# Optimization experiments

Hardware: AMD Instinct MI355X
Metric: run time of the kernel (lower is better)

The kernel has to match this reference:

```python
import jax, jax.numpy as jnp
import numpy as np
from jax import lax

EPS = 1e-5
NUM_BITS = 8          # activation quantization bits
NUM_BITS_WEIGHT = 8   # weight quantization bits


def fake_quant(x, bits):
    """Uniform min-max quantize-dequantize (per-tensor), STE on round."""
    mn = jnp.min(x)
    mx = jnp.max(x)
    scale = jnp.maximum((mx - mn) / (2 ** bits - 1), jnp.asarray(1e-8, x.dtype))
    q = jnp.round((x - mn) / scale) * scale + mn
    # straight-through estimator: identity gradient through rounding
    return x + lax.stop_gradient(q - x)


def batchnorm(x, gamma, beta, mean, var):
    # x: [N, C, H, W]; stats per channel C (eval mode, running stats)
    inv = gamma / jnp.sqrt(var + EPS)
    return x * inv[None, :, None, None] + (beta - mean * inv)[None, :, None, None]


def qconv(x, w, padding):
    xq = fake_quant(x, NUM_BITS)
    wq = fake_quant(w, NUM_BITS_WEIGHT)
    return lax.conv_general_dilated(
        xq, wq, window_strides=(1, 1), padding=padding,
        dimension_numbers=("NCHW", "OIHW", "NCHW"))


def setup_inputs() -> dict:
    key = jax.random.key(0)
    ks = jax.random.split(key, 8)
    C_in, bn_size, growth = 512, 4, 32
    C_mid = bn_size * growth  # 128
    N, H, W = 64, 28, 28
    x = jax.random.normal(ks[0], (N, C_in, H, W), dtype=jnp.float32)
    gamma1 = jax.random.uniform(ks[1], (C_in,), minval=0.5, maxval=1.5)
    beta1 = jax.random.normal(ks[2], (C_in,)) * 0.1
    mean1 = jax.random.normal(ks[3], (C_in,)) * 0.1
    var1 = jax.random.uniform(ks[4], (C_in,), minval=0.5, maxval=1.5)
    w1 = jax.random.normal(ks[5], (C_mid, C_in, 1, 1)) * (1.0 / np.sqrt(C_in))
    gamma2 = jax.random.uniform(ks[6], (C_mid,), minval=0.5, maxval=1.5)
    beta2 = jax.random.normal(ks[7], (C_mid,)) * 0.1
    mean2 = jax.random.normal(jax.random.fold_in(key, 10), (C_mid,)) * 0.1
    var2 = jax.random.uniform(jax.random.fold_in(key, 11), (C_mid,), minval=0.5, maxval=1.5)
    w2 = jax.random.normal(jax.random.fold_in(key, 12), (growth, C_mid, 3, 3)) * (1.0 / np.sqrt(C_mid * 9))
    return {"x": x, "gamma1": gamma1, "beta1": beta1, "mean1": mean1, "var1": var1,
            "w1": w1, "gamma2": gamma2, "beta2": beta2, "mean2": mean2, "var2": var2,
            "w2": w2}


def reference(x, gamma1, beta1, mean1, var1, w1, gamma2, beta2, mean2, var2, w2):
    h = jax.nn.relu(batchnorm(x, gamma1, beta1, mean1, var1))
    h = qconv(h, w1, padding=((0, 0), (0, 0)))            # 1x1 conv, 512 -> 128
    h = jax.nn.relu(batchnorm(h, gamma2, beta2, mean2, var2))
    h = qconv(h, w2, padding=((1, 1), (1, 1)))            # 3x3 conv, 128 -> 32
    # drop_rate == 0 -> dropout is identity
    return h
```

## Files before the change

kernel.cpp:

```cpp
#include <hip/hip_runtime.h>

typedef unsigned short u16;
typedef unsigned short u16x4 __attribute__((ext_vector_type(4)));
typedef unsigned short u16x8 __attribute__((ext_vector_type(8)));
typedef short bf16x8 __attribute__((ext_vector_type(8)));
typedef float f32x4 __attribute__((ext_vector_type(4)));

#define EPSF 1e-5f

#define C1   512
#define C2   128
#define C3   32
#define HH   28
#define WW   28
#define HW   784
#define NHW  50176
#define XELEMS 25690112

#define SCAN_BLOCKS 1024
#define KA_GRID     1027
#define CONV1_BLOCKS 392
#define CONV2_BLOCKS 784

#define WS_BN1I   64
#define WS_BN1B   2112
#define WS_BN2I   4160
#define WS_BN2B   4672
#define WS_WQ1    5376
#define WS_WQ2    136448
#define WS_P1     210176
#define WS_P2     226560
#define WS_H2     233472

__device__ __forceinline__ float bf2f(u16 u) { return __uint_as_float(((unsigned)u) << 16); }
__device__ __forceinline__ u16 f2bf(float f) {
  unsigned x = __float_as_uint(f);
  return (u16)((x + 0x7fffu + ((x >> 16) & 1u)) >> 16);
}
__device__ __forceinline__ float finz(float f) {
  unsigned u = __float_as_uint(f);
  return ((u & 0x7f800000u) == 0x7f800000u) ? 0.0f : f;
}

__device__ __forceinline__ void block_minmax(float& mn, float& mx) {
  for (int m = 32; m; m >>= 1) {
    mn = fminf(mn, __shfl_xor(mn, m));
    mx = fmaxf(mx, __shfl_xor(mx, m));
  }
  __shared__ float wmn[4], wmx[4];
  const int wv = threadIdx.x >> 6;
  if ((threadIdx.x & 63) == 0) { wmn[wv] = mn; wmx[wv] = mx; }
  __syncthreads();
  if (threadIdx.x == 0) {
    mn = fminf(fminf(wmn[0], wmn[1]), fminf(wmn[2], wmn[3]));
    mx = fmaxf(fmaxf(wmx[0], wmx[1]), fmaxf(wmx[2], wmx[3]));
  }
}

__global__ __launch_bounds__(256) void kA_kernel(
    const float* __restrict__ x, const float* g1, const float* be1,
    const float* m1, const float* v1, const float* w1,
    const float* g2, const float* be2, const float* m2, const float* v2,
    const float* w2, unsigned char* ws) {
  const int t = threadIdx.x;
  const int bid = blockIdx.x;
  float2* p1 = (float2*)(ws + WS_P1);
  u16* wq1 = (u16*)(ws + WS_WQ1);
  u16* wq2 = (u16*)(ws + WS_WQ2);
  __shared__ float bc[2];

  if (bid < SCAN_BLOCKS) {
    const int c = bid >> 1;
    const int n0 = (bid & 1) << 5;
    const f32x4* xb = (const f32x4*)x + ((size_t)n0 * C1 + c) * 196;
    float mn0 = 3.4e38f, mx0 = -3.4e38f, mn1 = 3.4e38f, mx1 = -3.4e38f;
    float mn2 = 3.4e38f, mx2 = -3.4e38f, mn3 = 3.4e38f, mx3 = -3.4e38f;
    auto P = [&](int j, float& mn, float& mx) {
      int s = j / 196;
      int g = j - s * 196;
      f32x4 v = xb[(size_t)s * (C1 * 196) + g];
      mn = fminf(mn, fminf(fminf(v[0], v[1]), fminf(v[2], v[3])));
      mx = fmaxf(mx, fmaxf(fmaxf(v[0], v[1]), fmaxf(v[2], v[3])));
    };
    int j = t;
    for (; j + 768 < 6272; j += 1024) {
      P(j, mn0, mx0); P(j + 256, mn1, mx1);
      P(j + 512, mn2, mx2); P(j + 768, mn3, mx3);
    }
    for (; j < 6272; j += 256) P(j, mn0, mx0);
    float mn = fminf(fminf(mn0, mn1), fminf(mn2, mn3));
    float mx = fmaxf(fmaxf(mx0, mx1), fmaxf(mx2, mx3));
    block_minmax(mn, mx);
    if (t == 0) {
      float inv = g1[c] / sqrtf(v1[c] + EPSF);
      float bb = be1[c] - m1[c] * inv;
      float lo = fmaxf(fmaf(mn, inv, bb), 0.0f);
      float hi = fmaxf(fmaf(mx, inv, bb), 0.0f);
      p1[bid] = make_float2(lo, hi);
    }
  } else if (bid == SCAN_BLOCKS) {
    const f32x4* w4 = (const f32x4*)w1;
    float mn = 3.4e38f, mx = -3.4e38f;
#pragma unroll 8
    for (int k = t; k < 16384; k += 256) {
      f32x4 v = w4[k];
#pragma unroll
      for (int j = 0; j < 4; j++) {
        float f = finz(v[j]); mn = fminf(mn, f); mx = fmaxf(mx, f);
      }
    }
    block_minmax(mn, mx);
    if (t == 0) { bc[0] = mn; bc[1] = mx; }
    __syncthreads();
    const float mnv = bc[0];
    const float s = fmaxf((bc[1] - mnv) / 255.0f, 1e-8f);
    const float rs = 1.0f / s;
#pragma unroll 4
    for (int k = t; k < 16384; k += 256) {
      f32x4 v = w4[k];
      u16x4 o;
#pragma unroll
      for (int j = 0; j < 4; j++)
        o[j] = f2bf(fmaf(rintf((finz(v[j]) - mnv) * rs), s, mnv));
      *(u16x4*)(wq1 + k * 4) = o;
    }
  } else if (bid == SCAN_BLOCKS + 1) {
    const f32x4* w4 = (const f32x4*)w2;
    float mn = 3.4e38f, mx = -3.4e38f;
#pragma unroll 4
    for (int k = t; k < 9216; k += 256) {
      f32x4 v = w4[k];
#pragma unroll
      for (int j = 0; j < 4; j++) {
        float f = finz(v[j]); mn = fminf(mn, f); mx = fmaxf(mx, f);
      }
    }
    block_minmax(mn, mx);
    if (t == 0) { bc[0] = mn; bc[1] = mx; }
    __syncthreads();
    const float mnv = bc[0];
    const float s = fmaxf((bc[1] - mnv) / 255.0f, 1e-8f);
    const float rs = 1.0f / s;
    for (int jj = t; jj < 36864; jj += 256) {
      int tap = jj >> 12;
      int rem = jj & 4095;
      float f = finz(w2[rem * 9 + tap]);
      wq2[jj] = f2bf(fmaf(rintf((f - mnv) * rs), s, mnv));
    }
  } else {
    float* bn1i = (float*)(ws + WS_BN1I);
    float* bn1b = (float*)(ws + WS_BN1B);
    float* bn2i = (float*)(ws + WS_BN2I);
    float* bn2b = (float*)(ws + WS_BN2B);
    for (int c = t; c < C1; c += 256) {
      float inv = g1[c] / sqrtf(v1[c] + EPSF);
      bn1i[c] = inv;
      bn1b[c] = be1[c] - m1[c] * inv;
    }
    if (t < C2) {
      float inv = g2[t] / sqrtf(v2[t] + EPSF);
      bn2i[t] = inv;
      bn2b[t] = be2[t] - m2[t] * inv;
    }
  }
}

__global__ __launch_bounds__(256) void conv1_kernel(const float* __restrict__ x,
                                                    unsigned char* ws) {
  const float* bn1i = (const float*)(ws + WS_BN1I);
  const float* bn1b = (const float*)(ws + WS_BN1B);
  const float* bn2i = (const float*)(ws + WS_BN2I);
  const float* bn2b = (const float*)(ws + WS_BN2B);
  const u16* wq1 = (const u16*)(ws + WS_WQ1);
  const float2* p1 = (const float2*)(ws + WS_P1);
  float2* p2 = (float2*)(ws + WS_P2);
  u16* h2 = (u16*)(ws + WS_H2);

  __shared__ __align__(16) u16 Alds[2][128 * 40];
  __shared__ __align__(16) u16 Blds[2][128 * 40];
  __shared__ float bc[2];
  __shared__ float wred[8];

  const int t = threadIdx.x;
  const int sp0 = blockIdx.x * 128;

  {
    float mn = 3.4e38f, mx = 0.0f;
    for (int i = t; i < SCAN_BLOCKS; i += 256) {
      float2 p = p1[i];
      mn = fminf(mn, p.x); mx = fmaxf(mx, p.y);
    }
    block_minmax(mn, mx);
    if (t == 0) { bc[0] = mn; bc[1] = mx; }
    __syncthreads();
  }
  const float mn1 = bc[0];
  const float s1 = fmaxf((bc[1] - mn1) / 255.0f, 1e-8f);
  const float r1 = 1.0f / s1;

  const int kk = t >> 3;
  const int spA = (t & 7) * 8;
  const int spB = 64 + spA;
  const int ga = sp0 + spA, gb = sp0 + spB;
  const int na = ga / HW, hwa = ga % HW;
  const int nb = gb / HW, hwb = gb % HW;
  const float* xA = x + na * (C1 * HW) + hwa;
  const float* xB = x + nb * (C1 * HW) + hwb;
  const int colg = (kk & 7) + 8 * ((((kk >> 3) + (spA >> 3))) & 3);

  const int wco = t >> 1;
  const int wko = (t & 1) * 16;
  const int ab0 = wko >> 3;
  const int aswz = (wco >> 3) & 3;

  const int lane = t & 63;
  const int l15 = lane & 15;
  const int q = lane >> 4;
  const int wv = t >> 6;
  const int wy = wv >> 1;
  const int wx = wv & 1;

  f32x4 acc[4][4] = {};

  u16x8 a0 = *(const u16x8*)(wq1 + wco * C1 + wko);
  u16x8 a1 = *(const u16x8*)(wq1 + wco * C1 + wko + 8);
  f32x4 va0 = *(const f32x4*)(xA + kk * HW);
  f32x4 va1 = *(const f32x4*)(xA + kk * HW + 4);
  f32x4 vb0 = *(const f32x4*)(xB + kk * HW);
  f32x4 vb1 = *(const f32x4*)(xB + kk * HW + 4);
  float inv = bn1i[kk], bb = bn1b[kk];

#pragma unroll 1
  for (int i = 0; i < 16; i++) {
    const int cur = i & 1;
    *(u16x8*)&Alds[cur][wco * 40 + (((ab0 + 0 + aswz) & 3) << 3)] = a0;
    *(u16x8*)&Alds[cur][wco * 40 + (((ab0 + 1 + aswz) & 3) << 3)] = a1;
#pragma unroll
    for (int j = 0; j < 4; j++) {
      float f0 = fmaxf(fmaf(va0[j], inv, bb), 0.0f);
      Blds[cur][(spA + j) * 40 + colg] = f2bf(fmaf(rintf((f0 - mn1) * r1), s1, mn1));
      float f1 = fmaxf(fmaf(va1[j], inv, bb), 0.0f);
      Blds[cur][(spA + 4 + j) * 40 + colg] = f2bf(fmaf(rintf((f1 - mn1) * r1), s1, mn1));
      float g0 = fmaxf(fmaf(vb0[j], inv, bb), 0.0f);
      Blds[cur][(spB + j) * 40 + colg] = f2bf(fmaf(rintf((g0 - mn1) * r1), s1, mn1));
      float g1v = fmaxf(fmaf(vb1[j], inv, bb), 0.0f);
      Blds[cur][(spB + 4 + j) * 40 + colg] = f2bf(fmaf(rintf((g1v - mn1) * r1), s1, mn1));
    }
    if (i < 15) {
      const int kn = (i + 1) * 32;
      a0 = *(const u16x8*)(wq1 + wco * C1 + kn + wko);
      a1 = *(const u16x8*)(wq1 + wco * C1 + kn + wko + 8);
      const int c = kn + kk;
      va0 = *(const f32x4*)(xA + c * HW);
      va1 = *(const f32x4*)(xA + c * HW + 4);
      vb0 = *(const f32x4*)(xB + c * HW);
      vb1 = *(const f32x4*)(xB + c * HW + 4);
      inv = bn1i[c]; bb = bn1b[c];
    }
    __syncthreads();
    bf16x8 af[4], bfr[4];
#pragma unroll
    for (int ii = 0; ii < 4; ii++) {
      int R = wy * 64 + ii * 16 + l15;
      af[ii] = *(const bf16x8*)&Alds[cur][R * 40 + (((q + (R >> 3)) & 3) << 3)];
    }
#pragma unroll
    for (int j = 0; j < 4; j++) {
      int R = wx * 64 + j * 16 + l15;
      bfr[j] = *(const bf16x8*)&Blds[cur][R * 40 + (((q + (R >> 3)) & 3) << 3)];
    }
#pragma unroll
    for (int ii = 0; ii < 4; ii++)
#pragma unroll
      for (int j = 0; j < 4; j++)
        acc[ii][j] = __builtin_amdgcn_mfma_f32_16x16x32_bf16(af[ii], bfr[j], acc[ii][j], 0, 0, 0);
  }

  float lmn = 3.4e38f, lmx = 0.0f;
#pragma unroll
  for (int i = 0; i < 4; i++) {
    int cob = wy * 64 + i * 16 + q * 4;
    f32x4 i2 = *(const f32x4*)&bn2i[cob];
    f32x4 b2 = *(const f32x4*)&bn2b[cob];
#pragma unroll
    for (int j = 0; j < 4; j++) {
      int sp = sp0 + wx * 64 + j * 16 + l15;
      u16x4 v;
#pragma unroll
      for (int r = 0; r < 4; r++) {
        float h = fmaxf(fmaf(acc[i][j][r], i2[r], b2[r]), 0.0f);
        v[r] = f2bf(h);
        lmn = fminf(lmn, h); lmx = fmaxf(lmx, h);
      }
      *(u16x4*)&h2[sp * C2 + cob] = v;
    }
  }
  for (int m = 32; m; m >>= 1) {
    lmn = fminf(lmn, __shfl_xor(lmn, m));
    lmx = fmaxf(lmx, __shfl_xor(lmx, m));
  }
  if (lane == 0) { wred[wv] = lmn; wred[4 + wv] = lmx; }
  __syncthreads();
  if (t == 0) {
    float2 pr;
    pr.x = fminf(fminf(wred[0], wred[1]), fminf(wred[2], wred[3]));
    pr.y = fmaxf(fmaxf(wred[4], wred[5]), fmaxf(wred[6], wred[7]));
    p2[blockIdx.x] = pr;
  }
}

__global__ __launch_bounds__(256) void conv2_kernel(const unsigned char* ws,
                                                    float* __restrict__ out) {
  const u16* wq2 = (const u16*)(ws + WS_WQ2);
  const u16* h2 = (const u16*)(ws + WS_H2);
  const float2* p2 = (const float2*)(ws + WS_P2);
  __shared__ float bc2[2];

  const int t = threadIdx.x;
  {
    float mn = 3.4e38f, mx = 0.0f;
    for (int i = t; i < CONV1_BLOCKS; i += 256) {
      float2 p = p2[i];
      mn = fminf(mn, p.x); mx = fmaxf(mx, p.y);
    }
    block_minmax(mn, mx);
    if (t == 0) { bc2[0] = mn; bc2[1] = mx; }
    __syncthreads();
  }
  const float mn2 = bc2[0];
  const float s2 = fmaxf((bc2[1] - mn2) / 255.0f, 1e-8f);
  const float r2 = 1.0f / s2;

  const int lane = t & 63;
  const int l15 = lane & 15;
  const int q = lane >> 4;
  const int wv = t >> 6;

  const int B = blockIdx.x;
  const int sblk = (B & 7) * 98 + (B >> 3);
  const int spf = sblk * 64 + wv * 16 + l15;
  const int nn = spf / HW;
  const int hwf = spf % HW;
  const int hf = hwf / WW;
  const int wf = hwf % WW;

  f32x4 acc[2] = {};
  bf16x8 bz;
#pragma unroll
  for (int j = 0; j < 8; j++) bz[j] = 0;

  for (int tap = 0; tap < 9; tap++) {
    const int dh = tap / 3 - 1, dw = tap % 3 - 1;
    const u16* wA = wq2 + tap * (C3 * C2);
    unsigned h2i = (unsigned)(hf + dh);
    unsigned w2i = (unsigned)(wf + dw);
    const bool val = (h2i < 28u) && (w2i < 28u);
    const u16* bptr = h2 + ((size_t)(nn * HW + (int)h2i * WW + (int)w2i)) * C2;
#pragma unroll
    for (int ks = 0; ks < C2; ks += 32) {
      bf16x8 a[2], b;
#pragma unroll
      for (int f = 0; f < 2; f++)
        a[f] = *(const bf16x8*)(wA + (f * 16 + l15) * C2 + ks + q * 8);
      if (val) {
        u16x8 hv = *(const u16x8*)(bptr + ks + q * 8);
#pragma unroll
        for (int j = 0; j < 8; j++) {
          float h = bf2f(hv[j]);
          b[j] = (short)f2bf(fmaf(rintf((h - mn2) * r2), s2, mn2));
        }
      } else {
        b = bz;
      }
#pragma unroll
      for (int i = 0; i < 2; i++)
        acc[i] = __builtin_amdgcn_mfma_f32_16x16x32_bf16(a[i], b, acc[i], 0, 0, 0);
    }
  }

#pragma unroll
  for (int i = 0; i < 2; i++) {
    int co = i * 16 + q * 4;
#pragma unroll
    for (int r = 0; r < 4; r++)
      out[(nn * C3 + co + r) * HW + hwf] = acc[i][r];
  }
}

extern "C" void kernel_launch(void* const* d_in, const int* in_sizes, int n_in,
                              void* d_out, int out_size, void* d_ws, size_t ws_size,
                              hipStream_t stream) {
  const float* x  = (const float*)d_in[0];
  const float* g1 = (const float*)d_in[1];
  const float* b1 = (const float*)d_in[2];
  const float* m1 = (const float*)d_in[3];
  const float* v1 = (const float*)d_in[4];
  const float* w1 = (const float*)d_in[5];
  const float* g2 = (const float*)d_in[6];
  const float* b2 = (const float*)d_in[7];
  const float* m2 = (const float*)d_in[8];
  const float* v2 = (const float*)d_in[9];
  const float* w2 = (const float*)d_in[10];
  unsigned char* ws = (unsigned char*)d_ws;
  float* out = (float*)d_out;

  kA_kernel<<<KA_GRID, 256, 0, stream>>>(x, g1, b1, m1, v1, w1, g2, b2, m2, v2, w2, ws);
  conv1_kernel<<<CONV1_BLOCKS, 256, 0, stream>>>(x, ws);
  conv2_kernel<<<CONV2_BLOCKS, 256, 0, stream>>>(ws, out);
}
```

Measured before the change: 262.4 us.

## Halve conv1 spatial tile to double block count; reorder kA blocks; vectorize w2 quant

Result: no change. 265.4 us (+1.1%).

```diff
diff --git a/kernel.cpp b/kernel.cpp
--- a/kernel.cpp
+++ b/kernel.cpp
@@ -15,11 +15,10 @@
 #define WW   28
 #define HW   784
 #define NHW  50176
-#define XELEMS 25690112
 
 #define SCAN_BLOCKS 1024
 #define KA_GRID     1027
-#define CONV1_BLOCKS 392
+#define CONV1_BLOCKS 784
 #define CONV2_BLOCKS 784
 
 #define WS_BN1I   64
@@ -69,9 +68,10 @@
   u16* wq2 = (u16*)(ws + WS_WQ2);
   __shared__ float bc[2];
 
-  if (bid < SCAN_BLOCKS) {
-    const int c = bid >> 1;
-    const int n0 = (bid & 1) << 5;
+  if (bid >= 3) {
+    const int sb = bid - 3;
+    const int c = sb >> 1;
+    const int n0 = (sb & 1) << 5;
     const f32x4* xb = (const f32x4*)x + ((size_t)n0 * C1 + c) * 196;
     float mn0 = 3.4e38f, mx0 = -3.4e38f, mn1 = 3.4e38f, mx1 = -3.4e38f;
     float mn2 = 3.4e38f, mx2 = -3.4e38f, mn3 = 3.4e38f, mx3 = -3.4e38f;
@@ -96,9 +96,9 @@
       float bb = be1[c] - m1[c] * inv;
       float lo = fmaxf(fmaf(mn, inv, bb), 0.0f);
       float hi = fmaxf(fmaf(mx, inv, bb), 0.0f);
-      p1[bid] = make_float2(lo, hi);
-    }
-  } else if (bid == SCAN_BLOCKS) {
+      p1[sb] = make_float2(lo, hi);
+    }
+  } else if (bid == 0) {
     const f32x4* w4 = (const f32x4*)w1;
     float mn = 3.4e38f, mx = -3.4e38f;
 #pragma unroll 8
@@ -124,7 +124,7 @@
         o[j] = f2bf(fmaf(rintf((finz(v[j]) - mnv) * rs), s, mnv));
       *(u16x4*)(wq1 + k * 4) = o;
     }
-  } else if (bid == SCAN_BLOCKS + 1) {
+  } else if (bid == 1) {
     const f32x4* w4 = (const f32x4*)w2;
     float mn = 3.4e38f, mx = -3.4e38f;
 #pragma unroll 4
@@ -141,11 +141,16 @@
     const float mnv = bc[0];
     const float s = fmaxf((bc[1] - mnv) / 255.0f, 1e-8f);
     const float rs = 1.0f / s;
-    for (int jj = t; jj < 36864; jj += 256) {
-      int tap = jj >> 12;
-      int rem = jj & 4095;
-      float f = finz(w2[rem * 9 + tap]);
-      wq2[jj] = f2bf(fmaf(rintf((f - mnv) * rs), s, mnv));
+    for (int k = t; k < 9216; k += 256) {
+      f32x4 v = w4[k];
+      int L = k * 4;
+#pragma unroll
+      for (int j = 0; j < 4; j++) {
+        int e = L + j;
+        int cc = e / 9;
+        int tap = e - cc * 9;
+        wq2[tap * 4096 + cc] = f2bf(fmaf(rintf((finz(v[j]) - mnv) * rs), s, mnv));
+      }
     }
   } else {
     float* bn1i = (float*)(ws + WS_BN1I);
@@ -177,12 +182,12 @@
   u16* h2 = (u16*)(ws + WS_H2);
 
   __shared__ __align__(16) u16 Alds[2][128 * 40];
-  __shared__ __align__(16) u16 Blds[2][128 * 40];
+  __shared__ __align__(16) u16 Blds[2][64 * 40];
   __shared__ float bc[2];
   __shared__ float wred[8];
 
   const int t = threadIdx.x;
-  const int sp0 = blockIdx.x * 128;
+  const int sp0 = blockIdx.x * 64;
 
   {
     float mn = 3.4e38f, mx = 0.0f;
@@ -200,12 +205,9 @@
 
   const int kk = t >> 3;
   const int spA = (t & 7) * 8;
-  const int spB = 64 + spA;
-  const int ga = sp0 + spA, gb = sp0 + spB;
+  const int ga = sp0 + spA;
   const int na = ga / HW, hwa = ga % HW;
-  const int nb = gb / HW, hwb = gb % HW;
   const float* xA = x + na * (C1 * HW) + hwa;
-  const float* xB = x + nb * (C1 * HW) + hwb;
   const int colg = (kk & 7) + 8 * ((((kk >> 3) + (spA >> 3))) & 3);
 
   const int wco = t >> 1;
@@ -217,17 +219,13 @@
   const int l15 = lane & 15;
   const int q = lane >> 4;
   const int wv = t >> 6;
-  const int wy = wv >> 1;
-  const int wx = wv & 1;
-
-  f32x4 acc[4][4] = {};
+
+  f32x4 acc[2][4] = {};
 
   u16x8 a0 = *(const u16x8*)(wq1 + wco * C1 + wko);
   u16x8 a1 = *(const u16x8*)(wq1 + wco * C1 + wko + 8);
   f32x4 va0 = *(const f32x4*)(xA + kk * HW);
   f32x4 va1 = *(const f32x4*)(xA + kk * HW + 4);
-  f32x4 vb0 = *(const f32x4*)(xB + kk * HW);
-  f32x4 vb1 = *(const f32x4*)(xB + kk * HW + 4);
   float inv = bn1i[kk], bb = bn1b[kk];
 
 #pragma unroll 1
@@ -241,10 +239,6 @@
       Blds[cur][(spA + j) * 40 + colg] = f2bf(fmaf(rintf((f0 - mn1) * r1), s1, mn1));
       float f1 = fmaxf(fmaf(va1[j], inv, bb), 0.0f);
       Blds[cur][(spA + 4 + j) * 40 + colg] = f2bf(fmaf(rintf((f1 - mn1) * r1), s1, mn1));
-      float g0 = fmaxf(fmaf(vb0[j], inv, bb), 0.0f);
-      Blds[cur][(spB + j) * 40 + colg] = f2bf(fmaf(rintf((g0 - mn1) * r1), s1, mn1));
-      float g1v = fmaxf(fmaf(vb1[j], inv, bb), 0.0f);
-      Blds[cur][(spB + 4 + j) * 40 + colg] = f2bf(fmaf(rintf((g1v - mn1) * r1), s1, mn1));
     }
     if (i < 15) {
       const int kn = (i + 1) * 32;
@@ -253,24 +247,22 @@
       const int c = kn + kk;
       va0 = *(const f32x4*)(xA + c * HW);
       va1 = *(const f32x4*)(xA + c * HW + 4);
-      vb0 = *(const f32x4*)(xB + c * HW);
-      vb1 = *(const f32x4*)(xB + c * HW + 4);
       inv = bn1i[c]; bb = bn1b[c];
     }
     __syncthreads();
-    bf16x8 af[4], bfr[4];
-#pragma unroll
-    for (int ii = 0; ii < 4; ii++) {
-      int R = wy * 64 + ii * 16 + l15;
+    bf16x8 af[2], bfr[4];
+#pragma unroll
+    for (int ii = 0; ii < 2; ii++) {
+      int R = wv * 32 + ii * 16 + l15;
       af[ii] = *(const bf16x8*)&Alds[cur][R * 40 + (((q + (R >> 3)) & 3) << 3)];
     }
 #pragma unroll
     for (int j = 0; j < 4; j++) {
-      int R = wx * 64 + j * 16 + l15;
+      int R = j * 16 + l15;
       bfr[j] = *(const bf16x8*)&Blds[cur][R * 40 + (((q + (R >> 3)) & 3) << 3)];
     }
 #pragma unroll
-    for (int ii = 0; ii < 4; ii++)
+    for (int ii = 0; ii < 2; ii++)
 #pragma unroll
       for (int j = 0; j < 4; j++)
         acc[ii][j] = __builtin_amdgcn_mfma_f32_16x16x32_bf16(af[ii], bfr[j], acc[ii][j], 0, 0, 0);
@@ -278,13 +270,13 @@
 
   float lmn = 3.4e38f, lmx = 0.0f;
 #pragma unroll
-  for (int i = 0; i < 4; i++) {
-    int cob = wy * 64 + i * 16 + q * 4;
+  for (int i = 0; i < 2; i++) {
+    int cob = wv * 32 + i * 16 + q * 4;
     f32x4 i2 = *(const f32x4*)&bn2i[cob];
     f32x4 b2 = *(const f32x4*)&bn2b[cob];
 #pragma unroll
     for (int j = 0; j < 4; j++) {
-      int sp = sp0 + wx * 64 + j * 16 + l15;
+      int sp = sp0 + j * 16 + l15;
       u16x4 v;
 #pragma unroll
       for (int r = 0; r < 4; r++) {
```
